# Kernel tuning notes

Measured on AMD Instinct MI355X. Metric: run time of the kernel, lower is better.

The kernel has to match this reference:

```python
import jax, jax.numpy as jnp
import numpy as np

EPS_NORM = 1e-8  # F.normalize eps (clamps norm from below)
EPS_ERR = 1e-8   # eps added under sqrt for the error


def _normalize(x, eps=EPS_NORM):
    n = jnp.linalg.norm(x, axis=-1, keepdims=True)
    return x / jnp.maximum(n, eps)


def _frame_basis(frames):
    """frames: [b, n, 3, 3]; points a, b, c are the COLUMNS (unbind dim=-1).
    Returns origin b_pt [b, n, 3] and orthonormal basis E [b, n, 3(basis k), 3(xyz d)]."""
    a, b_pt, c = frames[..., 0], frames[..., 1], frames[..., 2]
    w1 = _normalize(a - b_pt)
    w2 = _normalize(c - b_pt)
    e1 = _normalize(w1 + w2)
    e2 = _normalize(w2 - w1)
    e3 = jnp.cross(e1, e2)
    return b_pt, jnp.stack([e1, e2, e3], axis=-2)


def _pair_transform(coords, frames):
    """t[b,i,j,k] = dot(coords[b,i] - origin[b,j], E[b,j,k]).
    Exploits linearity to avoid materializing the [b,n,n,3] difference tensor."""
    origin, E = _frame_basis(frames)
    proj_c = jnp.einsum('bid,bjkd->bijk', coords, E)          # [b,n,n,3]
    proj_o = jnp.einsum('bjd,bjkd->bjk', origin, E)           # [b,n,3]
    return proj_c - proj_o[:, None, :, :]


def setup_inputs() -> dict:
    key = jax.random.key(0)
    k1, k2, k3, k4 = jax.random.split(key, 4)
    b, n = 2, 2048
    return {
        'pred_coords': jax.random.normal(k1, (b, n, 3), dtype=jnp.float32),
        'true_coords': jax.random.normal(k2, (b, n, 3), dtype=jnp.float32),
        'pred_frames': jax.random.normal(k3, (b, n, 3, 3), dtype=jnp.float32),
        'true_frames': jax.random.normal(k4, (b, n, 3, 3), dtype=jnp.float32),
    }


def reference(pred_coords, true_coords, pred_frames, true_frames):
    # coord index i is expressed in frame index j -> errors [b, n, n]
    t_pred = _pair_transform(pred_coords, pred_frames)
    t_true = _pair_transform(true_coords, true_frames)
    diff = t_pred - t_true
    return jnp.sqrt(jnp.sum(diff * diff, axis=-1) + EPS_ERR)
```

## Files before the change

### kernel.cpp

```cpp
#include <hip/hip_runtime.h>
#include <math.h>

#define EPS_NORM 1e-8f
#define EPS_ERR  1e-8f

__device__ inline void norm3(float& x, float& y, float& z) {
    float nn = sqrtf(x*x + y*y + z*z);
    float inv = 1.0f / fmaxf(nn, EPS_NORM);
    x *= inv; y *= inv; z *= inv;
}

__device__ inline void basis_from_frame(const float* __restrict__ F, size_t base,
                                        float* e , float* o ) {
    float ax = F[base + 0], bx = F[base + 1], cx = F[base + 2];
    float ay = F[base + 3], by = F[base + 4], cy = F[base + 5];
    float az = F[base + 6], bz = F[base + 7], cz = F[base + 8];
    float w1x = ax - bx, w1y = ay - by, w1z = az - bz;
    float w2x = cx - bx, w2y = cy - by, w2z = cz - bz;
    norm3(w1x, w1y, w1z);
    norm3(w2x, w2y, w2z);
    float e1x = w1x + w2x, e1y = w1y + w2y, e1z = w1z + w2z;
    float e2x = w2x - w1x, e2y = w2y - w1y, e2z = w2z - w1z;
    norm3(e1x, e1y, e1z);
    norm3(e2x, e2y, e2z);
    float e3x = e1y * e2z - e1z * e2y;
    float e3y = e1z * e2x - e1x * e2z;
    float e3z = e1x * e2y - e1y * e2x;
    e[0] = e1x; e[1] = e1y; e[2] = e1z;
    e[3] = e2x; e[4] = e2y; e[5] = e2z;
    e[6] = e3x; e[7] = e3y; e[8] = e3z;
    o[0] = bx * e1x + by * e1y + bz * e1z;
    o[1] = bx * e2x + by * e2y + bz * e2z;
    o[2] = bx * e3x + by * e3y + bz * e3z;
}

__global__ __launch_bounds__(256) void frames_kernel(
    const float* __restrict__ predF, const float* __restrict__ trueF,
    float* __restrict__ fd, int total_bn)
{
    int idx = blockIdx.x * 256 + threadIdx.x;
    if (idx >= total_bn) return;
    float e[9], o[3];
    float* dst = fd + (size_t)idx * 24;
    basis_from_frame(predF, (size_t)idx * 9, e, o);
    #pragma unroll
    for (int k = 0; k < 9; ++k) dst[k] = e[k];
    #pragma unroll
    for (int k = 0; k < 3; ++k) dst[9 + k] = o[k];
    basis_from_frame(trueF, (size_t)idx * 9, e, o);
    #pragma unroll
    for (int k = 0; k < 9; ++k) dst[12 + k] = e[k];
    #pragma unroll
    for (int k = 0; k < 3; ++k) dst[21 + k] = o[k];
}

template<int IT>
__global__ __launch_bounds__(256) void pair_err_kernel(
    const float* __restrict__ cp, const float* __restrict__ ct,
    const float* __restrict__ fd, float* __restrict__ out, int n)
{
    int j  = blockIdx.x * 256 + threadIdx.x;
    int bi = blockIdx.z;
    if (j >= n) return;

    const float4* f4 = reinterpret_cast<const float4*>(fd + ((size_t)bi * n + j) * 24);
    float4 q0 = f4[0], q1 = f4[1], q2 = f4[2], q3 = f4[3], q4 = f4[4], q5 = f4[5];
    const float ep0 = q0.x, ep1 = q0.y, ep2 = q0.z,
                ep3 = q0.w, ep4 = q1.x, ep5 = q1.y,
                ep6 = q1.z, ep7 = q1.w, ep8 = q2.x;
    const float op0 = q2.y, op1 = q2.z, op2 = q2.w;
    const float et0 = q3.x, et1 = q3.y, et2 = q3.z,
                et3 = q3.w, et4 = q4.x, et5 = q4.y,
                et6 = q4.z, et7 = q4.w, et8 = q5.x;
    const float ot0 = q5.y, ot1 = q5.z, ot2 = q5.w;

    const int i0 = blockIdx.y * IT;
    #pragma unroll
    for (int ii = 0; ii < IT; ++ii) {
        int i = i0 + ii;
        if (i >= n) break;
        size_t cbase = ((size_t)bi * n + i) * 3;
        float px = cp[cbase + 0], py = cp[cbase + 1], pz = cp[cbase + 2];
        float tx = ct[cbase + 0], ty = ct[cbase + 1], tz = ct[cbase + 2];
        float d0 = (px * ep0 + py * ep1 + pz * ep2 - op0) - (tx * et0 + ty * et1 + tz * et2 - ot0);
        float d1 = (px * ep3 + py * ep4 + pz * ep5 - op1) - (tx * et3 + ty * et4 + tz * et5 - ot1);
        float d2 = (px * ep6 + py * ep7 + pz * ep8 - op2) - (tx * et6 + ty * et7 + tz * et8 - ot2);
        out[((size_t)bi * n + i) * n + j] = sqrtf(d0 * d0 + d1 * d1 + d2 * d2 + EPS_ERR);
    }
}

extern "C" void kernel_launch(void* const* d_in, const int* in_sizes, int n_in,
                              void* d_out, int out_size, void* d_ws, size_t ws_size,
                              hipStream_t stream) {
    const float* pred_coords = (const float*)d_in[0];
    const float* true_coords = (const float*)d_in[1];
    const float* pred_frames = (const float*)d_in[2];
    const float* true_frames = (const float*)d_in[3];
    float* out = (float*)d_out;

    int total_bn = in_sizes[0] / 3;
    int n = (int)((long long)out_size / total_bn);
    int b = total_bn / n;

    float* fd = (float*)d_ws;

    int blocks1 = (total_bn + 255) / 256;
    frames_kernel<<<blocks1, 256, 0, stream>>>(pred_frames, true_frames, fd, total_bn);

    constexpr int IT = 8;
    dim3 grid((n + 255) / 256, (n + IT - 1) / IT, b);
    pair_err_kernel<IT><<<grid, 256, 0, stream>>>(pred_coords, true_coords, fd, out, n);
}
```

Measured before the change: 80.60 us.

## Store frame data in SoA layout, fold origin offsets, raise rows per block

The frame workspace is rewritten in structure-of-arrays form, so each of the 21 per-frame values is read coalesced across threads. The pred and true origin projections are folded into a single difference vector, which drops three values per frame. Each block now handles 32 output rows instead of 8, which amortizes the per-thread frame load over more outputs. The kernel is bound by output writes, so the gain is likely small, and the runtime-bounded loop with unroll 8 may add a little overhead.

```diff
diff --git a/kernel.cpp b/kernel.cpp
--- a/kernel.cpp
+++ b/kernel.cpp
@@ -40,52 +40,44 @@
 {
     int idx = blockIdx.x * 256 + threadIdx.x;
     if (idx >= total_bn) return;
-    float e[9], o[3];
-    float* dst = fd + (size_t)idx * 24;
-    basis_from_frame(predF, (size_t)idx * 9, e, o);
+    float ep[9], op[3], et[9], ot[3];
+    basis_from_frame(predF, (size_t)idx * 9, ep, op);
+    basis_from_frame(trueF, (size_t)idx * 9, et, ot);
     #pragma unroll
-    for (int k = 0; k < 9; ++k) dst[k] = e[k];
+    for (int k = 0; k < 9; ++k) fd[(size_t)k * total_bn + idx] = ep[k];
     #pragma unroll
-    for (int k = 0; k < 3; ++k) dst[9 + k] = o[k];
-    basis_from_frame(trueF, (size_t)idx * 9, e, o);
+    for (int k = 0; k < 9; ++k) fd[(size_t)(9 + k) * total_bn + idx] = et[k];
     #pragma unroll
-    for (int k = 0; k < 9; ++k) dst[12 + k] = e[k];
-    #pragma unroll
-    for (int k = 0; k < 3; ++k) dst[21 + k] = o[k];
+    for (int k = 0; k < 3; ++k) fd[(size_t)(18 + k) * total_bn + idx] = op[k] - ot[k];
 }
 
 template<int IT>
 __global__ __launch_bounds__(256) void pair_err_kernel(
     const float* __restrict__ cp, const float* __restrict__ ct,
-    const float* __restrict__ fd, float* __restrict__ out, int n)
+    const float* __restrict__ fd, float* __restrict__ out, int n, int total_bn)
 {
     int j  = blockIdx.x * 256 + threadIdx.x;
     int bi = blockIdx.z;
     if (j >= n) return;
+    int idx = bi * n + j;
 
-    const float4* f4 = reinterpret_cast<const float4*>(fd + ((size_t)bi * n + j) * 24);
-    float4 q0 = f4[0], q1 = f4[1], q2 = f4[2], q3 = f4[3], q4 = f4[4], q5 = f4[5];
-    const float ep0 = q0.x, ep1 = q0.y, ep2 = q0.z,
-                ep3 = q0.w, ep4 = q1.x, ep5 = q1.y,
-                ep6 = q1.z, ep7 = q1.w, ep8 = q2.x;
-    const float op0 = q2.y, op1 = q2.z, op2 = q2.w;
-    const float et0 = q3.x, et1 = q3.y, et2 = q3.z,
-                et3 = q3.w, et4 = q4.x, et5 = q4.y,
-                et6 = q4.z, et7 = q4.w, et8 = q5.x;
-    const float ot0 = q5.y, ot1 = q5.z, ot2 = q5.w;
+    float f[21];
+    #pragma unroll
+    for (int c = 0; c < 21; ++c) f[c] = fd[(size_t)c * total_bn + idx];
 
     const int i0 = blockIdx.y * IT;
-    #pragma unroll
-    for (int ii = 0; ii < IT; ++ii) {
-        int i = i0 + ii;
-        if (i >= n) break;
-        size_t cbase = ((size_t)bi * n + i) * 3;
-        float px = cp[cbase + 0], py = cp[cbase + 1], pz = cp[cbase + 2];
-        float tx = ct[cbase + 0], ty = ct[cbase + 1], tz = ct[cbase + 2];
-        float d0 = (px * ep0 + py * ep1 + pz * ep2 - op0) - (tx * et0 + ty * et1 + tz * et2 - ot0);
-        float d1 = (px * ep3 + py * ep4 + pz * ep5 - op1) - (tx * et3 + ty * et4 + tz * et5 - ot1);
-        float d2 = (px * ep6 + py * ep7 + pz * ep8 - op2) - (tx * et6 + ty * et7 + tz * et8 - ot2);
-        out[((size_t)bi * n + i) * n + j] = sqrtf(d0 * d0 + d1 * d1 + d2 * d2 + EPS_ERR);
+    const int iters = min(IT, n - i0);
+    size_t obase = ((size_t)bi * n + i0) * n + j;
+    size_t cbase = ((size_t)bi * n + i0) * 3;
+
+    #pragma unroll 8
+    for (int ii = 0; ii < iters; ++ii) {
+        float px = cp[cbase + ii * 3 + 0], py = cp[cbase + ii * 3 + 1], pz = cp[cbase + ii * 3 + 2];
+        float tx = ct[cbase + ii * 3 + 0], ty = ct[cbase + ii * 3 + 1], tz = ct[cbase + ii * 3 + 2];
+        float d0 = px * f[0] + py * f[1] + pz * f[2] - (tx * f[ 9] + ty * f[10] + tz * f[11]) - f[18];
+        float d1 = px * f[3] + py * f[4] + pz * f[5] - (tx * f[12] + ty * f[13] + tz * f[14]) - f[19];
+        float d2 = px * f[6] + py * f[7] + pz * f[8] - (tx * f[15] + ty * f[16] + tz * f[17]) - f[20];
+        out[obase + (size_t)ii * n] = sqrtf(d0 * d0 + d1 * d1 + d2 * d2 + EPS_ERR);
     }
 }
 
@@ -107,7 +99,7 @@
     int blocks1 = (total_bn + 255) / 256;
     frames_kernel<<<blocks1, 256, 0, stream>>>(pred_frames, true_frames, fd, total_bn);
 
-    constexpr int IT = 8;
+    constexpr int IT = 32;
     dim3 grid((n + 255) / 256, (n + IT - 1) / IT, b);
-    pair_err_kernel<IT><<<grid, 256, 0, stream>>>(pred_coords, true_coords, fd, out, n);
+    pair_err_kernel<IT><<<grid, 256, 0, stream>>>(pred_coords, true_coords, fd, out, n, total_bn);
 }
```

Result: slower. 84.08 us (+4.3%).
